# Kernel optimization log

Measured on AMD Instinct MI355X. Metric: run time of the kernel, lower is better.

The kernel has to match this reference:

```python
import jax, jax.numpy as jnp
import numpy as np
from jax import lax

B, T, D, H, O = 64, 2048, 512, 512, 512


def setup_inputs() -> dict:
    key = jax.random.key(0)
    ks = jax.random.split(key, 8)
    s_in = 1.0 / np.sqrt(D)
    s_h = 1.0 / np.sqrt(H)
    s_o = 1.0 / np.sqrt(O)
    return {
        "embeddings": jax.random.normal(ks[0], (B, T, D), dtype=jnp.float32),
        "last_logits": jax.random.normal(ks[1], (B, O), dtype=jnp.float32),
        "Whx": jax.random.normal(ks[2], (H, D), dtype=jnp.float32) * s_in,
        "bhx": jax.random.normal(ks[3], (H,), dtype=jnp.float32) * s_in,
        "Wyh": jax.random.normal(ks[4], (H, O), dtype=jnp.float32) * s_o,
        "byh": jax.random.normal(ks[5], (H,), dtype=jnp.float32) * s_o,
        "Wout": jax.random.normal(ks[6], (O, H), dtype=jnp.float32) * s_h,
        "bout": jax.random.normal(ks[7], (O,), dtype=jnp.float32) * s_h,
    }


def reference(embeddings, last_logits, Whx, bhx, Wyh, byh, Wout, bout):
    # Precompute the input projection for all timesteps in one big GEMM:
    # xh[b,t,h] = hx(x_t)  (time-parallel part of the Jordan cell)
    xh = jnp.einsum('btd,hd->bth', embeddings, Whx) + bhx  # [B,T,H]

    def step(y_t, xh_t):
        # h_t = tanh(hx(x_t) + yh(y_t)); y_t = lm_head(h_t)
        h = jnp.tanh(xh_t + y_t @ Wyh.T + byh)   # [B,H]
        y = h @ Wout.T + bout                    # [B,O]
        return y, y

    last, ys = lax.scan(step, last_logits, jnp.swapaxes(xh, 0, 1))  # scan over T
    logits = jnp.swapaxes(ys, 0, 1)  # [B,T,O]
    return logits, last
```

## Files before the change

### kernel.cpp

```cpp
#include <hip/hip_runtime.h>
#include <hip/hip_bf16.h>


#define NB 64
#define NT 2048
#define ND 512
#define NH 512
#define NO 512
#define TH (NT * NH)

typedef float f32x4 __attribute__((ext_vector_type(4)));
typedef __bf16 bf16x8 __attribute__((ext_vector_type(8)));
typedef unsigned short u16x8 __attribute__((ext_vector_type(8)));
typedef unsigned short u16x4 __attribute__((ext_vector_type(4)));

__device__ __forceinline__ unsigned short f2bf(float x) {
  unsigned u = __builtin_bit_cast(unsigned, x);
  u += 0x7FFFu + ((u >> 16) & 1u);
  return (unsigned short)(u >> 16);
}
__device__ __forceinline__ float bf2f(unsigned short u) {
  return __builtin_bit_cast(float, (unsigned)u << 16);
}
__device__ __forceinline__ bf16x8 ld_frag(const unsigned short* p) {
  u16x8 r = *(const u16x8*)p;
  return __builtin_bit_cast(bf16x8, r);
}
__device__ __forceinline__ f32x4 ld_frag4(const unsigned short* p) {
  return *(const f32x4*)p;
}
__device__ __forceinline__ float fast_tanh(float x) {
  float ax = __builtin_fabsf(x);
  float e = __builtin_amdgcn_exp2f(ax * 2.8853900817779268f);
  float r = 1.0f - 2.0f * __builtin_amdgcn_rcpf(e + 1.0f);
  return __builtin_copysignf(r, x);
}


__global__ void k_bias(const float* __restrict__ Wyh, const float* __restrict__ bout,
                       const float* __restrict__ bhx, const float* __restrict__ byh,
                       float* bias_t0, float* bias_t) {
  int j = threadIdx.x;
  const float* row = Wyh + j * NO;
  float acc = 0.f;
  for (int o = 0; o < NO; ++o) acc += row[o] * bout[o];
  bias_t0[j] = bhx[j] + byh[j];
  bias_t[j]  = bhx[j] + byh[j] + acc;
}

__global__ void k_z0(const float* __restrict__ ll, const float* __restrict__ Wyh,
                     float* z0) {
  int b = blockIdx.x, j = threadIdx.x;
  const float* row = Wyh + j * NO;
  const float* lr = ll + b * NO;
  float acc = 0.f;
  for (int o = 0; o < NO; ++o) acc += lr[o] * row[o];
  z0[b * NH + j] = acc;
}

__global__ void k_wc(const float* __restrict__ Wyh, const float* __restrict__ Wout,
                     float* Wc) {
  int j = blockIdx.x, k = threadIdx.x;
  float acc = 0.f;
  for (int o = 0; o < NO; ++o) acc += Wyh[j * NO + o] * Wout[o * NH + k];
  Wc[j * NH + k] = acc;
}

__global__ void k_frag(const float* __restrict__ src, unsigned short* __restrict__ dst) {
  int gid = blockIdx.x * 256 + threadIdx.x;
  int lane = gid & 63, tidx = gid >> 6;
  int nt = tidx & 31, kt = tidx >> 5;
  const float* s = src + (size_t)(nt * 16 + (lane & 15)) * 512 + kt * 32 + (lane >> 4) * 8;
  unsigned short* d = dst + (size_t)gid * 8;
#pragma unroll
  for (int i = 0; i < 8; ++i) d[i] = f2bf(s[i]);
}

__device__ __forceinline__ int pre_idx(int col) {
  int w = col >> 7;
  return w * 128 + ((w >> 1) << 9) + (col & 15) * 8 + ((col >> 4) & 7);
}

template <int MODE>
__global__ __launch_bounds__(512) void k_gemm(
    const void* __restrict__ Ain, const unsigned short* __restrict__ fragB,
    float* __restrict__ out, const float* __restrict__ bias_t0,
    const float* __restrict__ bias_t, const float* __restrict__ z0,
    const float* __restrict__ bout, float* __restrict__ last) {
  __shared__ __align__(16) unsigned short a_lds[64 * 512];
  int tid = threadIdx.x;
  long bt0 = (long)blockIdx.x * 64;

  if (MODE == 0) {
    const float* A = (const float*)Ain;
#pragma unroll
    for (int it = 0; it < 16; ++it) {
      int chunk = it * 512 + tid;
      int r = chunk >> 7, c4 = chunk & 127;
      float4 v = ((const float4*)A)[(bt0 + r) * 128 + c4];
      int idx = (r * 512 + c4 * 4) ^ ((r & 7) << 3);
      unsigned short* p = &a_lds[idx];
      p[0] = f2bf(v.x); p[1] = f2bf(v.y); p[2] = f2bf(v.z); p[3] = f2bf(v.w);
    }
  } else {
    const unsigned short* A = (const unsigned short*)Ain;
#pragma unroll
    for (int it = 0; it < 8; ++it) {
      int chunk = it * 512 + tid;
      int r = chunk >> 6, c8 = chunk & 63;
      u16x8 v = *(const u16x8*)(A + (size_t)(bt0 + r) * 1024 + 256 + c8 * 8);
      int idx = (r * 512 + c8 * 8) ^ ((r & 7) << 3);
      *(u16x8*)&a_lds[idx] = v;
    }
  }
  __syncthreads();

  int wave = tid >> 6, lane = tid & 63;
  int r0 = (wave & 3) * 16, c0 = (wave >> 2) * 256;
  f32x4 acc[16];
#pragma unroll
  for (int n = 0; n < 16; ++n) acc[n] = (f32x4){0.f, 0.f, 0.f, 0.f};
  int arow = r0 + (lane & 15);

  for (int kt = 0; kt < 16; ++kt) {
    int aidx = (arow * 512 + kt * 32 + (lane >> 4) * 8) ^ ((arow & 7) << 3);
    bf16x8 a = ld_frag(&a_lds[aidx]);
    const unsigned short* bp = fragB + ((size_t)(kt * 32 + (c0 >> 4)) * 64 + lane) * 8;
#pragma unroll
    for (int n = 0; n < 16; ++n) {
      bf16x8 b = ld_frag(bp + (size_t)n * 512);
      acc[n] = __builtin_amdgcn_mfma_f32_16x16x32_bf16(a, b, acc[n], 0, 0, 0);
    }
  }

#pragma unroll
  for (int n = 0; n < 16; ++n) {
    int col = c0 + n * 16 + (lane & 15);
#pragma unroll
    for (int reg = 0; reg < 4; ++reg) {
      long row = bt0 + r0 + (lane >> 4) * 4 + reg;
      float v = acc[n][reg];
      if (MODE == 0) {
        int t = (int)(row & (NT - 1));
        long b = row >> 11;
        v += (t == 0) ? (bias_t0[col] + z0[b * NH + col]) : bias_t[col];
        ((unsigned short*)out)[row * 1024 + pre_idx(col)] = f2bf(v);
      } else {
        v += bout[col];
        out[row * 512 + col] = v;
        if ((row & (NT - 1)) == NT - 1) last[(row >> 11) * 512 + col] = v;
      }
    }
  }
}

__global__ __launch_bounds__(512, 2) void k_scan(float* __restrict__ buf,
                                                 const unsigned short* __restrict__ fragWc) {
  __shared__ __align__(16) unsigned short h_lds[2][16 * 512];
  __shared__ __align__(16) unsigned short wc_lds[8 * 12 * 512];
  unsigned short* hbuf = (unsigned short*)buf;
  const int tid = threadIdx.x;
  const int b0 = blockIdx.x * 16;
  const int wave = tid >> 6, lane = tid & 63;
  const int arow = lane & 15, bb = lane >> 4;
  const int c0 = wave * 64;
  const int swz = (arow & 7) << 3;
  const int w2 = wave >> 1;
  const int poff = w2 * 128 + ((w2 >> 1) << 9) + arow * 8 + (wave & 1) * 4;

  const unsigned short* bW = fragWc + ((size_t)(wave * 4) * 64 + lane) * 8;

#pragma unroll
  for (int g = 0; g < 3; ++g)
#pragma unroll
    for (int n = 0; n < 4; ++n) {
      f32x4 v = ld_frag4(bW + (size_t)((13 + g) * 32 + n) * 512);
      *(f32x4*)&wc_lds[(size_t)((wave * 3 + g) * 4 + n) * 512 + lane * 8] = v;
    }

  f32x4 ba[9][4];
#pragma unroll
  for (int g = 0; g < 9; ++g)
#pragma unroll
    for (int n = 0; n < 4; ++n) ba[g][n] = ld_frag4(bW + (size_t)(g * 32 + n) * 512);
#pragma unroll
  for (int g = 0; g < 9; ++g)
#pragma unroll
    for (int n = 0; n < 4; ++n) asm volatile("" : "+a"(ba[g][n]));

  u16x4 pr[4];
#pragma unroll
  for (int r = 0; r < 4; ++r)
    pr[r] = *(const u16x4*)(hbuf + (size_t)(b0 + bb * 4 + r) * (size_t)(NT * 1024) + poff);
#pragma unroll
  for (int r = 0; r < 4; ++r)
#pragma unroll
    for (int n = 0; n < 4; ++n) {
      float h = fast_tanh(bf2f(pr[r][n]));
      unsigned short hb = f2bf(h);
      int b = bb * 4 + r, col = c0 + n * 16 + arow;
      hbuf[(size_t)(b0 + b) * (size_t)(NT * 1024) + 256 + col] = hb;
      h_lds[0][(b * 512 + col) ^ ((b & 7) << 3)] = hb;
    }

  const unsigned short* pPre[4];
  unsigned short* pSt[4];
#pragma unroll
  for (int r = 0; r < 4; ++r) {
    size_t base = (size_t)(b0 + bb * 4 + r) * (size_t)(NT * 1024) + 1024;
    pPre[r] = hbuf + base + poff;
    pSt[r]  = hbuf + base + 256 + c0 + arow;
  }
#pragma unroll
  for (int r = 0; r < 4; ++r) pr[r] = *(const u16x4*)pPre[r];

  bf16x8 q0[4], q1[4];
#pragma unroll
  for (int n = 0; n < 4; ++n) q0[n] = ld_frag(bW + (size_t)(9 * 32 + n) * 512);
#pragma unroll
  for (int n = 0; n < 4; ++n) q1[n] = ld_frag(bW + (size_t)(10 * 32 + n) * 512);

  __syncthreads();

#define AIDX(k) ((arow * 512 + (k) * 32 + bb * 8) ^ swz)
#define AGPR_STEP(G)                                                            \
  {                                                                             \
    bf16x8 a = ld_frag(hs + AIDX(G));                                           \
    _Pragma("unroll") for (int n = 0; n < 4; ++n)                               \
        acc[n] = __builtin_amdgcn_mfma_f32_16x16x32_bf16(                       \
            a, __builtin_bit_cast(bf16x8, ba[G][n]), acc[n], 0, 0, 0);          \
  }
#define STREAM_STEP(Q, KT, RKT)                                                 \
  {                                                                             \
    bf16x8 a = ld_frag(hs + AIDX(KT));                                          \
    _Pragma("unroll") for (int n = 0; n < 4; ++n)                               \
        acc[n] = __builtin_amdgcn_mfma_f32_16x16x32_bf16(a, Q[n], acc[n], 0, 0, 0); \
    _Pragma("unroll") for (int n = 0; n < 4; ++n)                               \
        Q[n] = ld_frag(bWs + (size_t)((RKT) * 32 + n) * 512);                   \
  }
#define LDS_STEP(G)                                                             \
  {                                                                             \
    bf16x8 a = ld_frag(hs + AIDX(13 + G));                                      \
    _Pragma("unroll") for (int n = 0; n < 4; ++n) {                             \
      bf16x8 b = ld_frag(&wc_lds[(size_t)((wave * 3 + (G)) * 4 + n) * 512 + lane * 8]); \
      acc[n] = __builtin_amdgcn_mfma_f32_16x16x32_bf16(a, b, acc[n], 0, 0, 0);  \
    }                                                                           \
  }

#pragma unroll 1
  for (int t = 1; t < NT; ++t) {
    const unsigned short* bWs = bW;
    asm volatile("" : "+v"(bWs));

    f32x4 acc[4];
#pragma unroll
    for (int n = 0; n < 4; ++n)
#pragma unroll
      for (int r = 0; r < 4; ++r) acc[n][r] = bf2f(pr[r][n]);

    const unsigned short* hs = h_lds[(t - 1) & 1];

    AGPR_STEP(0) AGPR_STEP(1) AGPR_STEP(2) AGPR_STEP(3)
    STREAM_STEP(q0, 9, 11)
    AGPR_STEP(4) AGPR_STEP(5) AGPR_STEP(6) AGPR_STEP(7)
    STREAM_STEP(q1, 10, 12)
    AGPR_STEP(8)
    LDS_STEP(0)
    STREAM_STEP(q0, 11, 9)
    LDS_STEP(1)
    STREAM_STEP(q1, 12, 10)
    LDS_STEP(2)

    if (t < NT - 1) {
#pragma unroll
      for (int r = 0; r < 4; ++r) {
        pPre[r] += 1024;
        pr[r] = *(const u16x4*)pPre[r];
      }
    }

    unsigned short* hdst = h_lds[t & 1];
#pragma unroll
    for (int n = 0; n < 4; ++n)
#pragma unroll
      for (int r = 0; r < 4; ++r) {
        int b = bb * 4 + r;
        float h = fast_tanh(acc[n][r]);
        unsigned short hb = f2bf(h);
        pSt[r][n * 16] = hb;
        hdst[(b * 512 + c0 + n * 16 + arow) ^ ((b & 7) << 3)] = hb;
      }
#pragma unroll
    for (int r = 0; r < 4; ++r) pSt[r] += 1024;

    asm volatile("s_waitcnt lgkmcnt(0)" ::: "memory");
    __builtin_amdgcn_s_barrier();
    asm volatile("" ::: "memory");
  }
#undef LDS_STEP
#undef STREAM_STEP
#undef AGPR_STEP
#undef AIDX
}

extern "C" void kernel_launch(void* const* d_in, const int* in_sizes, int n_in,
                              void* d_out, int out_size, void* d_ws, size_t ws_size,
                              hipStream_t stream) {
  const float* emb  = (const float*)d_in[0];
  const float* ll   = (const float*)d_in[1];
  const float* Whx  = (const float*)d_in[2];
  const float* bhx  = (const float*)d_in[3];
  const float* Wyh  = (const float*)d_in[4];
  const float* byh  = (const float*)d_in[5];
  const float* Wout = (const float*)d_in[6];
  const float* bout = (const float*)d_in[7];

  float* buf  = (float*)d_out;
  float* last = buf + (size_t)NB * NT * NO;

  char* ws = (char*)d_ws;
  unsigned short* fragWhx  = (unsigned short*)ws;
  unsigned short* fragWc   = (unsigned short*)(ws + (512 * 512 * 2));
  unsigned short* fragWout = (unsigned short*)(ws + 2 * (512 * 512 * 2));
  float* z0      = (float*)(ws + 3 * (512 * 512 * 2));
  float* bias_t0 = z0 + NB * NH;
  float* bias_t  = bias_t0 + NH;
  float* Wc_f32  = bias_t + NH;

  k_bias<<<1, 512, 0, stream>>>(Wyh, bout, bhx, byh, bias_t0, bias_t);
  k_z0<<<64, 512, 0, stream>>>(ll, Wyh, z0);
  k_wc<<<512, 512, 0, stream>>>(Wyh, Wout, Wc_f32);
  k_frag<<<128, 256, 0, stream>>>(Whx, fragWhx);
  k_frag<<<128, 256, 0, stream>>>(Wc_f32, fragWc);
  k_frag<<<128, 256, 0, stream>>>(Wout, fragWout);

  k_gemm<0><<<2048, 512, 0, stream>>>(emb, fragWhx, buf, bias_t0, bias_t, z0, bout, last);
  k_scan<<<4, 512, 0, stream>>>(buf, fragWc);
  k_gemm<1><<<2048, 512, 0, stream>>>(buf, fragWout, buf, bias_t0, bias_t, z0, bout, last);
}
```

Baseline: 7.774 ms.

## Coalesce hidden-state global stores via LDS and rebalance AGPR/streamed weight fragments

The per-step hidden state was written to global memory as scattered 2-byte stores from each MFMA lane. It is now read back from LDS one step later as 16-byte vectors per thread and stored coalesced, with a final flush after the loop. The register-resident weight groups drop from 9 to 7 and a third streamed fragment buffer is added. This frees registers for the new copy path but streams more weight data from global or L2 each step.

New measurement: 7.682 ms. No clear change (-1.2%).

```diff
diff --git a/kernel.cpp b/kernel.cpp
--- a/kernel.cpp
+++ b/kernel.cpp
@@ -178,13 +178,13 @@
       *(f32x4*)&wc_lds[(size_t)((wave * 3 + g) * 4 + n) * 512 + lane * 8] = v;
     }
 
-  f32x4 ba[9][4];
-#pragma unroll
-  for (int g = 0; g < 9; ++g)
+  f32x4 ba[7][4];
+#pragma unroll
+  for (int g = 0; g < 7; ++g)
 #pragma unroll
     for (int n = 0; n < 4; ++n) ba[g][n] = ld_frag4(bW + (size_t)(g * 32 + n) * 512);
 #pragma unroll
-  for (int g = 0; g < 9; ++g)
+  for (int g = 0; g < 7; ++g)
 #pragma unroll
     for (int n = 0; n < 4; ++n) asm volatile("" : "+a"(ba[g][n]));
 
@@ -197,28 +197,33 @@
 #pragma unroll
     for (int n = 0; n < 4; ++n) {
       float h = fast_tanh(bf2f(pr[r][n]));
-      unsigned short hb = f2bf(h);
       int b = bb * 4 + r, col = c0 + n * 16 + arow;
-      hbuf[(size_t)(b0 + b) * (size_t)(NT * 1024) + 256 + col] = hb;
-      h_lds[0][(b * 512 + col) ^ ((b & 7) << 3)] = hb;
+      h_lds[0][(b * 512 + col) ^ ((b & 7) << 3)] = f2bf(h);
     }
 
   const unsigned short* pPre[4];
-  unsigned short* pSt[4];
-#pragma unroll
-  for (int r = 0; r < 4; ++r) {
-    size_t base = (size_t)(b0 + bb * 4 + r) * (size_t)(NT * 1024) + 1024;
-    pPre[r] = hbuf + base + poff;
-    pSt[r]  = hbuf + base + 256 + c0 + arow;
-  }
+#pragma unroll
+  for (int r = 0; r < 4; ++r)
+    pPre[r] = hbuf + (size_t)(b0 + bb * 4 + r) * (size_t)(NT * 1024) + 1024 + poff;
 #pragma unroll
   for (int r = 0; r < 4; ++r) pr[r] = *(const u16x4*)pPre[r];
 
-  bf16x8 q0[4], q1[4];
-#pragma unroll
-  for (int n = 0; n < 4; ++n) q0[n] = ld_frag(bW + (size_t)(9 * 32 + n) * 512);
-#pragma unroll
-  for (int n = 0; n < 4; ++n) q1[n] = ld_frag(bW + (size_t)(10 * 32 + n) * 512);
+  const int bA = tid >> 6, c8A = tid & 63;
+  const int bB = bA + 8;
+  const int ldsA = (bA * 512 + c8A * 8) ^ ((bA & 7) << 3);
+  const int ldsB = (bB * 512 + c8A * 8) ^ ((bB & 7) << 3);
+  unsigned short* pHA =
+      hbuf + (size_t)(b0 + bA) * (size_t)(NT * 1024) + 256 + c8A * 8;
+  unsigned short* pHB =
+      hbuf + (size_t)(b0 + bB) * (size_t)(NT * 1024) + 256 + c8A * 8;
+
+  bf16x8 q0[4], q1[4], q2[4];
+#pragma unroll
+  for (int n = 0; n < 4; ++n) q0[n] = ld_frag(bW + (size_t)(7 * 32 + n) * 512);
+#pragma unroll
+  for (int n = 0; n < 4; ++n) q1[n] = ld_frag(bW + (size_t)(8 * 32 + n) * 512);
+#pragma unroll
+  for (int n = 0; n < 4; ++n) q2[n] = ld_frag(bW + (size_t)(9 * 32 + n) * 512);
 
   __syncthreads();
 
@@ -252,24 +257,33 @@
     const unsigned short* bWs = bW;
     asm volatile("" : "+v"(bWs));
 
+    const unsigned short* hs = h_lds[(t - 1) & 1];
+
+    {
+      u16x8 hA = *(const u16x8*)&hs[ldsA];
+      u16x8 hB = *(const u16x8*)&hs[ldsB];
+      *(u16x8*)pHA = hA;
+      *(u16x8*)pHB = hB;
+      pHA += 1024; pHB += 1024;
+    }
+
     f32x4 acc[4];
 #pragma unroll
     for (int n = 0; n < 4; ++n)
 #pragma unroll
       for (int r = 0; r < 4; ++r) acc[n][r] = bf2f(pr[r][n]);
 
-    const unsigned short* hs = h_lds[(t - 1) & 1];
-
     AGPR_STEP(0) AGPR_STEP(1) AGPR_STEP(2) AGPR_STEP(3)
-    STREAM_STEP(q0, 9, 11)
-    AGPR_STEP(4) AGPR_STEP(5) AGPR_STEP(6) AGPR_STEP(7)
-    STREAM_STEP(q1, 10, 12)
-    AGPR_STEP(8)
+    AGPR_STEP(4) AGPR_STEP(5) AGPR_STEP(6)
+    STREAM_STEP(q0, 7, 10)
+    STREAM_STEP(q1, 8, 11)
+    STREAM_STEP(q2, 9, 12)
     LDS_STEP(0)
-    STREAM_STEP(q0, 11, 9)
+    STREAM_STEP(q0, 10, 7)
     LDS_STEP(1)
-    STREAM_STEP(q1, 12, 10)
+    STREAM_STEP(q1, 11, 8)
     LDS_STEP(2)
+    STREAM_STEP(q2, 12, 9)
 
     if (t < NT - 1) {
 #pragma unroll
@@ -286,16 +300,20 @@
       for (int r = 0; r < 4; ++r) {
         int b = bb * 4 + r;
         float h = fast_tanh(acc[n][r]);
-        unsigned short hb = f2bf(h);
-        pSt[r][n * 16] = hb;
-        hdst[(b * 512 + c0 + n * 16 + arow) ^ ((b & 7) << 3)] = hb;
+        hdst[(b * 512 + c0 + n * 16 + arow) ^ ((b & 7) << 3)] = f2bf(h);
       }
-#pragma unroll
-    for (int r = 0; r < 4; ++r) pSt[r] += 1024;
 
     asm volatile("s_waitcnt lgkmcnt(0)" ::: "memory");
     __builtin_amdgcn_s_barrier();
     asm volatile("" ::: "memory");
+  }
+
+  {
+    const unsigned short* hs = h_lds[(NT - 1) & 1];
+    u16x8 hA = *(const u16x8*)&hs[ldsA];
+    u16x8 hB = *(const u16x8*)&hs[ldsB];
+    *(u16x8*)pHA = hA;
+    *(u16x8*)pHB = hB;
   }
 #undef LDS_STEP
 #undef STREAM_STEP
```
